# Performance work log

Measured on AMD Instinct MI355X. Metric: run time of the kernel, lower is better.

## Reference

```python
import jax, jax.numpy as jnp
import numpy as np

N = 100000      # nodes
E = 1000000     # edges (before self loops)
F_IN = 128      # num_features
G = 512         # graphs in batch
NC = 10         # num_classes
EPS_BN = 1e-5
NEG_SLOPE = 0.2


def setup_inputs() -> dict:
    key = jax.random.key(0)
    ks = iter(jax.random.split(key, 40))
    rn = lambda shape, s=0.1: jax.random.normal(next(ks), shape, jnp.float32) * s
    inp = {
        "x": jax.random.normal(next(ks), (N, F_IN), jnp.float32),
        "edge_index": jax.random.randint(next(ks), (2, E), 0, N),
        "batch": jnp.sort(jax.random.randint(next(ks), (N,), 0, G)),
        "W1": rn((F_IN, 128)), "as1": rn((8, 16)), "ad1": rn((8, 16)), "b1": jnp.zeros((128,), jnp.float32),
        "g1": jnp.ones((128,), jnp.float32), "be1": jnp.zeros((128,), jnp.float32),
        "Wl1": rn((128, 16)), "bl1": jnp.zeros((16,), jnp.float32),
        "gl1": jnp.ones((16,), jnp.float32), "bel1": jnp.zeros((16,), jnp.float32),
        "W2": rn((16, 96)), "as2": rn((4, 24)), "ad2": rn((4, 24)), "b2": jnp.zeros((96,), jnp.float32),
        "g2": jnp.ones((96,), jnp.float32), "be2": jnp.zeros((96,), jnp.float32),
        "Wl2": rn((96, 24)), "bl2": jnp.zeros((24,), jnp.float32),
        "gl2": jnp.ones((24,), jnp.float32), "bel2": jnp.zeros((24,), jnp.float32),
        "W3": rn((24, 64)), "as3": rn((2, 32)), "ad3": rn((2, 32)), "b3": jnp.zeros((64,), jnp.float32),
        "g3": jnp.ones((64,), jnp.float32), "be3": jnp.zeros((64,), jnp.float32),
        # final classifier
        "Wo": rn((64, NC)), "bo": jnp.zeros((NC,), jnp.float32),
    }
    return inp


def _bn(h, gamma, beta):
    # training-mode BatchNorm1d: batch statistics, biased variance
    m = jnp.mean(h, axis=0)
    v = jnp.var(h, axis=0)
    return gamma * (h - m) * jax.lax.rsqrt(v + EPS_BN) + beta


def _gat(h_in, src, dst, W, a_src, a_dst, bias, n):
    heads, ch = a_src.shape
    h = (h_in @ W).reshape(n, heads, ch)                     # [N,H,C]
    alpha_s = jnp.sum(h * a_src, axis=-1)                    # [N,H]
    alpha_d = jnp.sum(h * a_dst, axis=-1)                    # [N,H]
    e = jax.nn.leaky_relu(alpha_s[src] + alpha_d[dst], NEG_SLOPE)   # [E,H]
    emax = jax.ops.segment_max(e, dst, num_segments=n)       # segment softmax over target
    e = jnp.exp(e - emax[dst])
    denom = jax.ops.segment_sum(e, dst, num_segments=n)
    alpha = e / (denom[dst] + 1e-16)                         # [E,H]
    msg = h[src] * alpha[:, :, None]                         # [E,H,C]
    out = jax.ops.segment_sum(msg, dst, num_segments=n)      # [N,H,C]
    return out.reshape(n, heads * ch) + bias


def reference(x, edge_index, batch,
              W1, as1, ad1, b1, g1, be1, Wl1, bl1, gl1, bel1,
              W2, as2, ad2, b2, g2, be2, Wl2, bl2, gl2, bel2,
              W3, as3, ad3, b3, g3, be3, Wo, bo):
    n = x.shape[0]
    loop = jnp.arange(n)
    src = jnp.concatenate([edge_index[0], loop])   # add self loops (PyG default)
    dst = jnp.concatenate([edge_index[1], loop])

    h = jax.nn.relu(_bn(_gat(x, src, dst, W1, as1, ad1, b1, n), g1, be1))
    h = jax.nn.relu(_bn(h @ Wl1 + bl1, gl1, bel1))
    h = jax.nn.relu(_bn(_gat(h, src, dst, W2, as2, ad2, b2, n), g2, be2))
    h = jax.nn.relu(_bn(h @ Wl2 + bl2, gl2, bel2))
    h = jax.nn.relu(_bn(_gat(h, src, dst, W3, as3, ad3, b3, n), g3, be3))

    # global mean pool over graphs
    counts = jax.ops.segment_sum(jnp.ones((n,), h.dtype), batch, num_segments=G)
    pooled = jax.ops.segment_sum(h, batch, num_segments=G) / jnp.maximum(counts, 1.0)[:, None]
    # dropout is identity in eval
    return pooled @ Wo + bo
```

## Files before the change

### kernel.cpp

```cpp
#include <hip/hip_runtime.h>

typedef unsigned short u16;
typedef unsigned int   u32;
typedef unsigned long long u64;
typedef __attribute__((ext_vector_type(8))) short short8;
typedef __attribute__((ext_vector_type(4))) float f32x4;

#define DEVI __device__ __forceinline__

#define NPB 256
#define SHB 8
#define BHB 64
#define PST 256
#define LOG2E 1.44269504088896340736f

DEVI float bf2f(u16 u){ union{u32 i; float f;} x; x.i = ((u32)u)<<16; return x.f; }
DEVI u16 f2bf(float f){ union{float f; u32 i;} x; x.f = f;
  u32 r = (x.i + 0x7FFFu + ((x.i>>16)&1u))>>16; return (u16)r; }
DEVI float lrelu(float x){ return x > 0.f ? x : 0.2f*x; }
DEVI float exp2g(float x){ return __builtin_amdgcn_exp2f(x); }
DEVI float gload(const void* p, size_t i, int f32){
  return f32 ? ((const float*)p)[i] : bf2f(((const u16*)p)[i]);
}

__global__ __launch_bounds__(256) void k_init(const void* x, int* flag){
  if (blockIdx.x == 0 && threadIdx.x == 0){
    const u16* p = (const u16*)x;
    int hits = 0;
    for (int j = 0; j < 512; j++){
      u16 e = (p[j] >> 7) & 0xFF;
      if (e >= 0xC0) hits++;
    }
    *flag = hits ? 1 : 0;
  }
}

__global__ __launch_bounds__(1024) void k_bhist(const int* ei, int E, int* hist, int NB){
  __shared__ int lh[512];
  for (int b = threadIdx.x; b < NB; b += 1024) lh[b] = 0;
  __syncthreads();
  for (int e = blockIdx.x*1024 + threadIdx.x; e < E; e += BHB*1024)
    atomicAdd(&lh[((u32)ei[E + e]) >> SHB], 1);
  __syncthreads();
  for (int b = threadIdx.x; b < NB; b += 1024) hist[blockIdx.x*NB + b] = lh[b];
}

__global__ __launch_bounds__(512) void k_bmid(int* hist, int* base, int* coff, int NB, int N){
  __shared__ int l[512];
  int t = threadIdx.x;
  int s = 0;
  if (t < NB){ for (int j = 0; j < BHB; j++) s += hist[j*NB + t]; }
  l[t] = s; __syncthreads();
  for (int st = 1; st < 512; st <<= 1){
    int a = (t >= st) ? l[t - st] : 0;
    __syncthreads();
    l[t] += a;
    __syncthreads();
  }
  int run0 = l[t] - s;
  if (t < NB){
    base[t] = run0;
    int run = run0;
    for (int j = 0; j < BHB; j++){ int v = hist[j*NB + t]; hist[j*NB + t] = run; run += v; }
  }
  if (t == 511){ base[NB] = l[511]; coff[N] = l[511]; }
}

__global__ __launch_bounds__(1024) void k_bfill(const int* ei, int E, const int* hist,
                                                u64* tmp, int NB){
  __shared__ int cur[512];
  for (int b = threadIdx.x; b < NB; b += 1024) cur[b] = hist[blockIdx.x*NB + b];
  __syncthreads();
  for (int e = blockIdx.x*1024 + threadIdx.x; e < E; e += BHB*1024){
    int s = ei[e], d = ei[E + e];
    int p = atomicAdd(&cur[((u32)d) >> SHB], 1);
    tmp[p] = ((u64)(u32)d << 32) | (u32)s;
  }
}

__global__ __launch_bounds__(256) void k_cfill(const u64* tmp, const int* base,
                                               int* coff, int* csr, int N){
  __shared__ int cnt[NPB], start[NPB];
  int b = blockIdx.x, t = threadIdx.x;
  int p0 = base[b], p1 = base[b + 1];
  cnt[t] = 0;
  __syncthreads();
  for (int i = p0 + t; i < p1; i += 256)
    atomicAdd(&cnt[(int)(tmp[i] >> 32) & (NPB - 1)], 1);
  __syncthreads();
  if (t == 0){
    int run = p0;
    for (int j = 0; j < NPB; j++){ start[j] = run; run += cnt[j]; }
  }
  __syncthreads();
  {
    int node = b*NPB + t;
    if (node < N) coff[node] = start[t];
    cnt[t] = 0;
  }
  __syncthreads();
  for (int i = p0 + t; i < p1; i += 256){
    u64 pr = tmp[i];
    int dj = (int)(pr >> 32) & (NPB - 1);
    int r = atomicAdd(&cnt[dj], 1);
    csr[start[dj] + r] = (int)(u32)pr;
  }
}

__global__ __launch_bounds__(256) void k_prepW(const void* Wg, u16* Wt, const int* dflag){
  const int f32 = dflag[0];
  for (int i = blockIdx.x*256 + threadIdx.x; i < 128*128; i += gridDim.x*256){
    int k = i >> 7, nn = i & 127;
    Wt[nn*128 + k] = f2bf(gload(Wg, i, f32));
  }
}

__global__ __launch_bounds__(256) void k_mfma1(const void* x, const u16* __restrict__ Wt,
                                               u16* __restrict__ out, int n, const int* dflag){
  const int f32 = dflag[0];
  const int wave = threadIdx.x >> 6;
  const int lane = threadIdx.x & 63;
  const int l15 = lane & 15, q = lane >> 4;
  const int arow = blockIdx.x*64 + wave*16 + l15;
  const bool rok = arow < n;

  f32x4 acc[8];
  #pragma unroll
  for (int t = 0; t < 8; t++) acc[t] = {0.f, 0.f, 0.f, 0.f};

  #pragma unroll
  for (int kk = 0; kk < 4; kk++){
    short8 a = {0,0,0,0,0,0,0,0};
    if (rok){
      const int ko = kk*32 + q*8;
      if (f32){
        const float* xp = (const float*)x + (size_t)arow*128 + ko;
        float4 v0 = *(const float4*)xp;
        float4 v1 = *(const float4*)(xp + 4);
        a[0]=(short)f2bf(v0.x); a[1]=(short)f2bf(v0.y); a[2]=(short)f2bf(v0.z); a[3]=(short)f2bf(v0.w);
        a[4]=(short)f2bf(v1.x); a[5]=(short)f2bf(v1.y); a[6]=(short)f2bf(v1.z); a[7]=(short)f2bf(v1.w);
      } else {
        a = *(const short8*)((const u16*)x + (size_t)arow*128 + ko);
      }
    }
    #pragma unroll
    for (int t = 0; t < 8; t++){
      short8 b = *(const short8*)(Wt + (size_t)(l15 + 16*t)*128 + kk*32 + q*8);
      acc[t] = __builtin_amdgcn_mfma_f32_16x16x32_bf16(a, b, acc[t], 0, 0, 0);
    }
  }

  const int orow0 = blockIdx.x*64 + wave*16 + q*4;
  #pragma unroll
  for (int r = 0; r < 4; r++){
    int orow = orow0 + r;
    if (orow < n){
      #pragma unroll
      for (int t = 0; t < 8; t++)
        out[(size_t)orow*128 + l15 + 16*t] = f2bf(acc[t][r]);
    }
  }
}

__global__ __launch_bounds__(256) void k_alpha1(const u16* __restrict__ A, const void* a_s, const void* a_d,
    u16* als, u16* ald, int n, const int* dflag){
  const int f32 = dflag[0];
  int idx = blockIdx.x*256 + threadIdx.x;
  if (idx >= n*8) return;
  int r = idx >> 3, hd = idx & 7;
  const u16* p = A + (size_t)r*128 + hd*16;
  float s = 0.f, d = 0.f;
  #pragma unroll
  for (int c = 0; c < 16; c++){
    float v = bf2f(p[c]);
    s = fmaf(v, gload(a_s, hd*16 + c, f32), s);
    d = fmaf(v, gload(a_d, hd*16 + c, f32), d);
  }
  als[idx] = f2bf(s * LOG2E); ald[idx] = f2bf(d * LOG2E);
}

template<int K,int M,int H,int RT,int TPB,bool AFFINE,bool ALPHA>
__global__ __launch_bounds__(TPB) void k_gemm(
    const u16* in, const void* Wg,
    const float* stat, const void* gam, const void* bet, float invn,
    const void* a_s, const void* a_d, u16* out, u16* als, u16* ald, int n,
    const int* dflag)
{
  constexpr int CT = 4;
  constexpr int TC = M/CT;
  constexpr int TR = TPB/TC;
  constexpr int ROWS = TR*RT;
  constexpr int C = M/H;
  static_assert(TPB % TC == 0, "");
  __shared__ __align__(16) u16 Wl[K*M];
  __shared__ float Il[ROWS*(K+1)];
  __shared__ float red[ALPHA ? (2*ROWS*TC) : 1];
  __shared__ float faL[AFFINE ? K : 1], fdL[AFFINE ? K : 1];

  const int f32 = dflag[0];
  if constexpr (AFFINE){
    for (int k = threadIdx.x; k < K; k += TPB){
      float m = stat[k]*invn;
      float vv = stat[128 + k]*invn - m*m;
      float a = gload(gam, k, f32) * rsqrtf(vv + 1e-5f);
      faL[k] = a;
      fdL[k] = gload(bet, k, f32) - m*a;
    }
    __syncthreads();
  }

  for (int i = threadIdx.x; i < K*M; i += TPB)
    Wl[i] = f32 ? f2bf(((const float*)Wg)[i]) : ((const u16*)Wg)[i];

  const int rowbase = blockIdx.x * ROWS;
  for (int i = threadIdx.x; i < ROWS*K; i += TPB){
    int rr = i / K, k = i - rr*K;
    int r = rowbase + rr;
    float v = 0.f;
    if (r < n){
      v = bf2f(in[(size_t)r*K + k]);
      if constexpr (AFFINE) v = fmaxf(fmaf(faL[k], v, fdL[k]), 0.f);
    }
    Il[rr*(K+1) + k] = v;
  }
  __syncthreads();

  const int tc = threadIdx.x % TC;
  const int tr = threadIdx.x / TC;
  float acc[RT][CT];
  #pragma unroll
  for (int j = 0; j < RT; j++)
    #pragma unroll
    for (int c = 0; c < CT; c++) acc[j][c] = 0.f;

  #pragma unroll 8
  for (int k = 0; k < K; k++){
    ushort4 u = *(const ushort4*)&Wl[k*M + tc*CT];
    float w0 = bf2f(u.x), w1 = bf2f(u.y), w2 = bf2f(u.z), w3 = bf2f(u.w);
    #pragma unroll
    for (int j = 0; j < RT; j++){
      float iv = Il[(tr + j*TR)*(K+1) + k];
      acc[j][0] = fmaf(iv, w0, acc[j][0]);
      acc[j][1] = fmaf(iv, w1, acc[j][1]);
      acc[j][2] = fmaf(iv, w2, acc[j][2]);
      acc[j][3] = fmaf(iv, w3, acc[j][3]);
    }
  }

  #pragma unroll
  for (int j = 0; j < RT; j++){
    int r = rowbase + tr + j*TR;
    if (r < n){
      ushort4 st;
      st.x = f2bf(acc[j][0]); st.y = f2bf(acc[j][1]);
      st.z = f2bf(acc[j][2]); st.w = f2bf(acc[j][3]);
      *(ushort4*)&out[(size_t)r*M + tc*CT] = st;
    }
  }

  if constexpr (ALPHA){
    #pragma unroll
    for (int j = 0; j < RT; j++){
      float ps = 0.f, pd = 0.f;
      #pragma unroll
      for (int c = 0; c < CT; c++){
        ps = fmaf(acc[j][c], gload(a_s, tc*CT + c, f32), ps);
        pd = fmaf(acc[j][c], gload(a_d, tc*CT + c, f32), pd);
      }
      red[(tr + j*TR)*TC + tc] = ps;
      red[ROWS*TC + (tr + j*TR)*TC + tc] = pd;
    }
    __syncthreads();
    if (threadIdx.x < ROWS){
      int r = rowbase + threadIdx.x;
      if (r < n){
        float hs[H], hd[H];
        #pragma unroll
        for (int h = 0; h < H; h++){ hs[h] = 0.f; hd[h] = 0.f; }
        for (int t2 = 0; t2 < TC; t2++){
          int hh = (t2*CT)/C;
          hs[hh] += red[threadIdx.x*TC + t2];
          hd[hh] += red[ROWS*TC + threadIdx.x*TC + t2];
        }
        #pragma unroll
        for (int h = 0; h < H; h++){
          als[(size_t)r*H + h] = f2bf(hs[h] * LOG2E);
          ald[(size_t)r*H + h] = f2bf(hd[h] * LOG2E);
        }
      }
    }
  }
}

template<int H,int C>
__global__ __launch_bounds__(256) void k_pullW(const u16* __restrict__ h,
    const u16* __restrict__ als, const u16* __restrict__ ald,
    const int* __restrict__ off, const int* __restrict__ csr, u16* __restrict__ out, int n)
{
  constexpr int F = H*C;
  constexpr int L = F/2;
  constexpr int LOGH = (H==8)?3:((H==4)?2:1);
  constexpr int EPG = 64 >> LOGH;
  int wid = blockIdx.x*4 + (threadIdx.x >> 6);
  if (wid >= n) return;
  int lane = threadIdx.x & 63;
  int uu = lane >> LOGH;
  int hh = lane & (H-1);
  int fl = (lane < L) ? lane : (L-1);
  int hd = (2*fl)/C;
  const u32* hw = (const u32*)h;

  float adw = bf2f(ald[(u32)wid*H + hh]);
  float wsw = exp2g(lrelu(bf2f(als[(u32)wid*H + hh]) + adw));
  float den_lane = (uu == 0) ? wsw : 0.f;

  float wsf = exp2g(lrelu(bf2f(als[(u32)wid*H + hd]) + bf2f(ald[(u32)wid*H + hd])));
  u32 vs = hw[(u32)wid*L + fl];
  float acc0 = wsf * bf2f((u16)vs);
  float acc1 = wsf * bf2f((u16)(vs >> 16));

  int e0 = off[wid], e1 = off[wid + 1];
  for (int e = e0; e < e1; e += EPG){
    int rem = e1 - e;
    int su = csr[e + (uu < rem ? uu : 0)];
    float w = exp2g(lrelu(bf2f(als[(u32)su*H + hh]) + adw));
    if (uu >= rem) w = 0.f;
    den_lane += w;
    int cnt = rem < EPG ? rem : EPG;
    for (int jj = 0; jj < cnt; jj += 8){
      int sb[8]; float wb[8]; u32 vv[8];
      #pragma unroll
      for (int j = 0; j < 8; j++){
        int sl = ((jj + j) << LOGH) + hd;
        sb[j] = __shfl(su, sl);
        wb[j] = __shfl(w,  sl);
      }
      #pragma unroll
      for (int j = 0; j < 8; j++) vv[j] = hw[(u32)sb[j]*L + fl];
      #pragma unroll
      for (int j = 0; j < 8; j++){
        acc0 = fmaf(wb[j], bf2f((u16)vv[j]), acc0);
        acc1 = fmaf(wb[j], bf2f((u16)(vv[j] >> 16)), acc1);
      }
    }
  }
  #pragma unroll
  for (int st = H; st < 64; st <<= 1) den_lane += __shfl_xor(den_lane, st);
  float den = __shfl(den_lane, hd);
  float r = 1.f/(den + 1e-16f);
  if (lane < L)
    ((u32*)out)[(u32)wid*L + fl] = (u32)f2bf(acc0*r) | ((u32)f2bf(acc1*r) << 16);
}

template<int F,int TPB>
__global__ __launch_bounds__(TPB) void k_statA(const u16* __restrict__ x, int n,
                                               float* __restrict__ part)
{
  constexpr int L = F/2;
  constexpr int RPB = TPB/L;
  static_assert(TPB % L == 0, "");
  int c = threadIdx.x % L;
  int tr = threadIdx.x / L;
  const u32* xw = (const u32*)x;
  int chunk = (n + (int)gridDim.x - 1)/(int)gridDim.x;
  int r0 = blockIdx.x*chunk;
  int r1 = r0 + chunk; if (r1 > n) r1 = n;
  float a0=0.f, a1=0.f, b0=0.f, b1=0.f;
  int r = r0 + tr;
  for (; r + 3*RPB < r1; r += 4*RPB){
    u32 v0 = xw[(size_t)r*L + c];
    u32 v1 = xw[(size_t)(r + RPB)*L + c];
    u32 v2 = xw[(size_t)(r + 2*RPB)*L + c];
    u32 v3 = xw[(size_t)(r + 3*RPB)*L + c];
    float f0 = bf2f((u16)v0), f1 = bf2f((u16)(v0 >> 16));
    float f2 = bf2f((u16)v1), f3 = bf2f((u16)(v1 >> 16));
    float f4 = bf2f((u16)v2), f5 = bf2f((u16)(v2 >> 16));
    float f6 = bf2f((u16)v3), f7 = bf2f((u16)(v3 >> 16));
    a0 += (f0 + f2) + (f4 + f6);
    a1 += (f1 + f3) + (f5 + f7);
    b0 += (f0*f0 + f2*f2) + (f4*f4 + f6*f6);
    b1 += (f1*f1 + f3*f3) + (f5*f5 + f7*f7);
  }
  for (; r < r1; r += RPB){
    u32 v = xw[(size_t)r*L + c];
    float f0 = bf2f((u16)v), f1 = bf2f((u16)(v >> 16));
    a0 += f0; b0 = fmaf(f0, f0, b0);
    a1 += f1; b1 = fmaf(f1, f1, b1);
  }
  __shared__ float l0[TPB], l1[TPB], l2[TPB], l3[TPB];
  l0[threadIdx.x] = a0; l1[threadIdx.x] = a1;
  l2[threadIdx.x] = b0; l3[threadIdx.x] = b1;
  __syncthreads();
  for (int t2 = threadIdx.x; t2 < 256; t2 += TPB){
    int col = t2 & 127;
    float s = 0.f;
    if (col < F){
      int cc = col >> 1, par = col & 1;
      const float* base = (t2 >= 128) ? (par ? l3 : l2) : (par ? l1 : l0);
      #pragma unroll 4
      for (int j = 0; j < RPB; j++) s += base[j*L + cc];
    }
    part[(size_t)blockIdx.x*256 + t2] = s;
  }
}

__global__ __launch_bounds__(256) void k_statB(const float* __restrict__ part,
                                               float* __restrict__ out, int P)
{
  int t = threadIdx.x;
  float s = 0.f;
  int b = 0;
  for (; b + 3 < P; b += 4)
    s += (part[(size_t)b*256 + t] + part[(size_t)(b+1)*256 + t])
       + (part[(size_t)(b+2)*256 + t] + part[(size_t)(b+3)*256 + t]);
  for (; b < P; b++) s += part[(size_t)b*256 + t];
  out[t] = s;
}

__global__ __launch_bounds__(256) void k_pool(const u16* B, const int* batch, int n,
    const float* stat, const void* g3, const void* be3, float invn,
    const void* Wo, const void* bo, void* outp, const int* dflag)
{
  const int f32 = dflag[0];
  __shared__ float fa[64], fd[64];
  if (threadIdx.x < 64){
    int k = threadIdx.x;
    float m = stat[k]*invn;
    float v = stat[128 + k]*invn - m*m;
    float a = gload(g3, k, f32) * rsqrtf(v + 1e-5f);
    fa[k] = a;
    fd[k] = gload(be3, k, f32) - m*a;
  }
  __syncthreads();

  int g = blockIdx.x;
  int lane = threadIdx.x & 63, wv = threadIdx.x >> 6;
  int s, e;
  { int l = 0, h = n; while (l < h){ int m = (l+h)>>1; if (batch[m] <  g) l = m+1; else h = m; } s = l; }
  { int l = s, h = n; while (l < h){ int m = (l+h)>>1; if (batch[m] <= g) l = m+1; else h = m; } e = l; }
  float a = fa[lane], d = fd[lane], acc = 0.f;
  for (int r = s + wv; r < e; r += 4)
    acc += fmaxf(fmaf(a, bf2f(B[(size_t)r*64 + lane]), d), 0.f);
  __shared__ float pl[4][64];
  pl[wv][lane] = acc;
  __syncthreads();
  if (wv == 0){
    float cnt = (e > s) ? (float)(e - s) : 1.f;
    pl[0][lane] = (pl[0][lane] + pl[1][lane] + pl[2][lane] + pl[3][lane]) / cnt;
  }
  __syncthreads();
  if (threadIdx.x < 10){
    int lo = threadIdx.x;
    float o = gload(bo, lo, f32);
    for (int l2 = 0; l2 < 64; l2++) o = fmaf(pl[0][l2], gload(Wo, l2*10 + lo, f32), o);
    if (f32) ((float*)outp)[g*10 + lo] = o;
    else     ((u16*) outp)[g*10 + lo] = f2bf(o);
  }
}

extern "C" void kernel_launch(void* const* d_in, const int* in_sizes, int n_in,
                              void* d_out, int out_size, void* d_ws, size_t ws_size,
                              hipStream_t stream)
{
  const void* x   = d_in[0];
  const int* ei   = (const int*)d_in[1];
  const int* batch= (const int*)d_in[2];
  const void* W1  = d_in[3];
  const void* as1 = d_in[4];
  const void* ad1 = d_in[5];
  const void* g1  = d_in[7];
  const void* be1 = d_in[8];
  const void* Wl1 = d_in[9];
  const void* gl1 = d_in[11];
  const void* bel1= d_in[12];
  const void* W2  = d_in[13];
  const void* as2 = d_in[14];
  const void* ad2 = d_in[15];
  const void* g2  = d_in[17];
  const void* be2 = d_in[18];
  const void* Wl2 = d_in[19];
  const void* gl2 = d_in[21];
  const void* bel2= d_in[22];
  const void* W3  = d_in[23];
  const void* as3 = d_in[24];
  const void* ad3 = d_in[25];
  const void* g3  = d_in[27];
  const void* be3 = d_in[28];
  const void* Wo  = d_in[29];
  const void* bo  = d_in[30];
  (void)n_in; (void)ws_size;

  const int N = in_sizes[2];
  const int E = in_sizes[1] / 2;
  const int G = out_size / 10;
  const int NB = (N + NPB - 1) >> SHB;

  char* w = (char*)d_ws;
  size_t off = 0;
  auto alloc = [&](size_t bytes)->void*{
    size_t o = off; off += (bytes + 255) & ~(size_t)255; return (void*)(w + o);
  };
  int*   dflag= (int*)alloc(4);
  int*   coff = (int*)alloc((size_t)(N+1)*4);
  int*   csr  = (int*)alloc((size_t)E*4);
  int*   bbase= (int*)alloc((size_t)(NB+1)*4);
  int*   hist = (int*)alloc((size_t)BHB*NB*4);
  float* stS  = (float*)alloc(1280*4);
  float* part = (float*)alloc((size_t)PST*256*4);
  u16*   Wt   = (u16*)alloc(128*128*2);
  u16*   als  = (u16*)alloc((size_t)N*8*2);
  u16*   ald  = (u16*)alloc((size_t)N*8*2);
  u16*   Cb   = (u16*)alloc((size_t)N*24*2);
  u16*   A    = (u16*)alloc((size_t)N*128*2);
  u16*   B    = (u16*)alloc((size_t)N*128*2);
  u64*   tmp  = (u64*)A;

  const float invN = 1.f/(float)N;

  k_init<<<1, 256, 0, stream>>>(x, dflag);
  k_prepW<<<16, 256, 0, stream>>>(W1, Wt, dflag);

  k_bhist<<<BHB, 1024, 0, stream>>>(ei, E, hist, NB);
  k_bmid <<<1, 512, 0, stream>>>(hist, bbase, coff, NB, N);
  k_bfill<<<BHB, 1024, 0, stream>>>(ei, E, hist, tmp, NB);
  k_cfill<<<NB, 256, 0, stream>>>(tmp, bbase, coff, csr, N);

  k_mfma1<<<(N+63)/64, 256, 0, stream>>>(x, Wt, A, N, dflag);
  k_alpha1<<<(N*8+255)/256, 256, 0, stream>>>(A, as1, ad1, als, ald, N, dflag);
  k_pullW<8,16><<<(N+3)/4, 256, 0, stream>>>(A, als, ald, coff, csr, B, N);
  k_statA<128,256><<<PST, 256, 0, stream>>>(B, N, part);
  k_statB<<<1, 256, 0, stream>>>(part, stS + 0, PST);

  k_gemm<128,16,1,1,256,true,false><<<(N+63)/64, 256, 0, stream>>>(
      B, Wl1, stS + 0, g1, be1, invN, nullptr, nullptr, Cb, nullptr, nullptr, N, dflag);
  k_statA<16,256><<<PST, 256, 0, stream>>>(Cb, N, part);
  k_statB<<<1, 256, 0, stream>>>(part, stS + 256, PST);

  k_gemm<16,96,4,2,192,true,true><<<(N+15)/16, 192, 0, stream>>>(
      Cb, W2, stS + 256, gl1, bel1, invN, as2, ad2, A, als, ald, N, dflag);
  k_pullW<4,24><<<(N+3)/4, 256, 0, stream>>>(A, als, ald, coff, csr, B, N);
  k_statA<96,192><<<PST, 192, 0, stream>>>(B, N, part);
  k_statB<<<1, 256, 0, stream>>>(part, stS + 512, PST);

  k_gemm<96,24,1,2,192,true,false><<<(N+63)/64, 192, 0, stream>>>(
      B, Wl2, stS + 512, g2, be2, invN, nullptr, nullptr, Cb, nullptr, nullptr, N, dflag);
  k_statA<24,192><<<PST, 192, 0, stream>>>(Cb, N, part);
  k_statB<<<1, 256, 0, stream>>>(part, stS + 768, PST);

  k_gemm<24,64,2,2,256,true,true><<<(N+31)/32, 256, 0, stream>>>(
      Cb, W3, stS + 768, gl2, bel2, invN, as3, ad3, A, als, ald, N, dflag);
  k_pullW<2,32><<<(N+3)/4, 256, 0, stream>>>(A, als, ald, coff, csr, B, N);
  k_statA<64,256><<<PST, 256, 0, stream>>>(B, N, part);
  k_statB<<<1, 256, 0, stream>>>(part, stS + 1024, PST);

  k_pool<<<G, 256, 0, stream>>>(B, batch, N, stS + 1024, g3, be3, invN, Wo, bo, d_out, dflag);
}
```

Before: 720.4 us.

## Aggregate GAT layers 2-3 before projection and parallelize CSR scan and stat reduction

For GAT layers 2 and 3, the attention logits are now computed from the low-dimensional input by folding a_src/a_dst into W (precomputed vectors). Neighbour aggregation runs on the 16- or 24-wide BN-activated input per head, and a block-diagonal weight GEMM is applied afterwards. This shrinks the gathered feature width per edge (64 or 48 values instead of 96 or 64). It also splits the single-block bucket scan into parallel total, scan and cursor kernels, and widens the final stat reduction to 1024 threads. The cost is extra kernel launches and a different rounding order from aggregating before the projection.

```diff
diff --git a/kernel.cpp b/kernel.cpp
--- a/kernel.cpp
+++ b/kernel.cpp
@@ -23,8 +23,8 @@
   return f32 ? ((const float*)p)[i] : bf2f(((const u16*)p)[i]);
 }
 
-__global__ __launch_bounds__(256) void k_init(const void* x, int* flag){
-  if (blockIdx.x == 0 && threadIdx.x == 0){
+__global__ __launch_bounds__(64) void k_init(const void* x, int* flag){
+  if (threadIdx.x == 0){
     const u16* p = (const u16*)x;
     int hits = 0;
     for (int j = 0; j < 512; j++){
@@ -45,25 +45,41 @@
   for (int b = threadIdx.x; b < NB; b += 1024) hist[blockIdx.x*NB + b] = lh[b];
 }
 
-__global__ __launch_bounds__(512) void k_bmid(int* hist, int* base, int* coff, int NB, int N){
+__global__ __launch_bounds__(256) void k_btot(const int* hist, int* tot, int NB){
+  int b = blockIdx.x*256 + threadIdx.x;
+  if (b < NB){
+    int s = 0;
+    #pragma unroll 8
+    for (int j = 0; j < BHB; j++) s += hist[j*NB + b];
+    tot[b] = s;
+  }
+}
+
+__global__ __launch_bounds__(512) void k_bscan(const int* tot, int* base, int* coff, int NB, int N){
   __shared__ int l[512];
   int t = threadIdx.x;
-  int s = 0;
-  if (t < NB){ for (int j = 0; j < BHB; j++) s += hist[j*NB + t]; }
-  l[t] = s; __syncthreads();
+  int v = (t < NB) ? tot[t] : 0;
+  l[t] = v; __syncthreads();
   for (int st = 1; st < 512; st <<= 1){
     int a = (t >= st) ? l[t - st] : 0;
     __syncthreads();
     l[t] += a;
     __syncthreads();
   }
-  int run0 = l[t] - s;
-  if (t < NB){
-    base[t] = run0;
-    int run = run0;
-    for (int j = 0; j < BHB; j++){ int v = hist[j*NB + t]; hist[j*NB + t] = run; run += v; }
-  }
+  if (t < NB) base[t] = l[t] - v;
   if (t == 511){ base[NB] = l[511]; coff[N] = l[511]; }
+}
+
+__global__ __launch_bounds__(256) void k_bcur(int* hist, const int* base, int NB){
+  int b = blockIdx.x*256 + threadIdx.x;
+  if (b < NB){
+    int run = base[b];
+    for (int j = 0; j < BHB; j++){
+      int v = hist[j*NB + b];
+      hist[j*NB + b] = run;
+      run += v;
+    }
+  }
 }
 
 __global__ __launch_bounds__(1024) void k_bfill(const int* ei, int E, const int* hist,
@@ -112,6 +128,46 @@
   for (int i = blockIdx.x*256 + threadIdx.x; i < 128*128; i += gridDim.x*256){
     int k = i >> 7, nn = i & 127;
     Wt[nn*128 + k] = f2bf(gload(Wg, i, f32));
+  }
+}
+
+__global__ __launch_bounds__(256) void k_prep23(const void* W2, const void* as2, const void* ad2,
+    const void* W3, const void* as3, const void* ad3,
+    u16* Wbd2, u16* Wbd3, float* prepF, const int* dflag){
+  const int f32 = dflag[0];
+  int t = threadIdx.x;
+  for (int i = t; i < 64*96; i += 256){
+    int r = i/96, m = i - r*96;
+    int h = r >> 4, k = r & 15;
+    float v = ((m/24) == h) ? gload(W2, k*96 + m, f32) : 0.f;
+    Wbd2[i] = f2bf(v);
+  }
+  for (int i = t; i < 48*64; i += 256){
+    int r = i >> 6, m = i & 63;
+    int h = r/24, k = r - h*24;
+    float v = ((m >> 5) == h) ? gload(W3, k*64 + m, f32) : 0.f;
+    Wbd3[i] = f2bf(v);
+  }
+  if (t < 64){
+    int h = t >> 4, k = t & 15;
+    float s = 0.f, d = 0.f;
+    for (int c = 0; c < 24; c++){
+      float w = gload(W2, k*96 + h*24 + c, f32);
+      s = fmaf(w, gload(as2, h*24 + c, f32), s);
+      d = fmaf(w, gload(ad2, h*24 + c, f32), d);
+    }
+    prepF[t] = s; prepF[64 + t] = d;
+  }
+  if (t >= 64 && t < 112){
+    int u = t - 64;
+    int h = u/24, k = u - h*24;
+    float s = 0.f, d = 0.f;
+    for (int c = 0; c < 32; c++){
+      float w = gload(W3, k*64 + h*32 + c, f32);
+      s = fmaf(w, gload(as3, h*32 + c, f32), s);
+      d = fmaf(w, gload(ad3, h*32 + c, f32), d);
+    }
+    prepF[128 + u] = s; prepF[176 + u] = d;
   }
 }
 
@@ -179,7 +235,7 @@
   als[idx] = f2bf(s * LOG2E); ald[idx] = f2bf(d * LOG2E);
 }
 
-template<int K,int M,int H,int RT,int TPB,bool AFFINE,bool ALPHA>
+template<int K,int M,int H,int RT,int TPB,bool AFFINE,bool ALPHA,bool WBF16>
 __global__ __launch_bounds__(TPB) void k_gemm(
     const u16* in, const void* Wg,
     const float* stat, const void* gam, const void* bet, float invn,
@@ -209,8 +265,10 @@
     __syncthreads();
   }
 
-  for (int i = threadIdx.x; i < K*M; i += TPB)
-    Wl[i] = f32 ? f2bf(((const float*)Wg)[i]) : ((const u16*)Wg)[i];
+  for (int i = threadIdx.x; i < K*M; i += TPB){
+    if constexpr (WBF16) Wl[i] = ((const u16*)Wg)[i];
+    else Wl[i] = f32 ? f2bf(((const float*)Wg)[i]) : ((const u16*)Wg)[i];
+  }
 
   const int rowbase = blockIdx.x * ROWS;
   for (int i = threadIdx.x; i < ROWS*K; i += TPB){
@@ -350,6 +408,90 @@
   float r = 1.f/(den + 1e-16f);
   if (lane < L)
     ((u32*)out)[(u32)wid*L + fl] = (u32)f2bf(acc0*r) | ((u32)f2bf(acc1*r) << 16);
+}
+
+template<int H,int CIN>
+__global__ __launch_bounds__(256) void k_alphaX(const u16* __restrict__ Cb,
+    const float* stat, const void* gam, const void* bet, float invn,
+    const float* vs, const float* vd,
+    u16* act, u16* als, u16* ald, int n, const int* dflag)
+{
+  const int f32 = dflag[0];
+  __shared__ float faL[CIN], fdL[CIN];
+  if (threadIdx.x < CIN){
+    int k = threadIdx.x;
+    float m = stat[k]*invn;
+    float vv = stat[128 + k]*invn - m*m;
+    float a = gload(gam, k, f32) * rsqrtf(vv + 1e-5f);
+    faL[k] = a;
+    fdL[k] = gload(bet, k, f32) - m*a;
+  }
+  __syncthreads();
+  int idx = blockIdx.x*256 + threadIdx.x;
+  if (idx >= n*H) return;
+  int j = idx / H, h = idx - j*H;
+  float s = 0.f, d = 0.f;
+  #pragma unroll
+  for (int k = 0; k < CIN; k++){
+    float v = bf2f(Cb[(size_t)j*CIN + k]);
+    v = fmaxf(fmaf(faL[k], v, fdL[k]), 0.f);
+    s = fmaf(v, vs[h*CIN + k], s);
+    d = fmaf(v, vd[h*CIN + k], d);
+    if (h == 0) act[(size_t)j*CIN + k] = f2bf(v);
+  }
+  als[idx] = f2bf(s * LOG2E); ald[idx] = f2bf(d * LOG2E);
+}
+
+template<int H,int CIN>
+__global__ __launch_bounds__(256) void k_pullX(const u16* __restrict__ act,
+    const u16* __restrict__ als, const u16* __restrict__ ald,
+    const int* __restrict__ off, const int* __restrict__ csr, u16* __restrict__ D, int n)
+{
+  constexpr int LX = H*CIN;
+  constexpr int LOGH = (H==4)?2:1;
+  constexpr int EPG = 64 >> LOGH;
+  int wid = blockIdx.x*4 + (threadIdx.x >> 6);
+  if (wid >= n) return;
+  int lane = threadIdx.x & 63;
+  int uu = lane >> LOGH;
+  int hh = lane & (H-1);
+  int fl = (lane < LX) ? lane : (LX-1);
+  int hf = fl / CIN, k = fl - hf*CIN;
+
+  float adw = bf2f(ald[(u32)wid*H + hh]);
+  float wsw = exp2g(lrelu(bf2f(als[(u32)wid*H + hh]) + adw));
+  float den_lane = (uu == 0) ? wsw : 0.f;
+
+  float wsf = exp2g(lrelu(bf2f(als[(u32)wid*H + hf]) + bf2f(ald[(u32)wid*H + hf])));
+  float acc = wsf * bf2f(act[(u32)wid*CIN + k]);
+
+  int e0 = off[wid], e1 = off[wid + 1];
+  for (int e = e0; e < e1; e += EPG){
+    int rem = e1 - e;
+    int su = csr[e + (uu < rem ? uu : 0)];
+    float w = exp2g(lrelu(bf2f(als[(u32)su*H + hh]) + adw));
+    if (uu >= rem) w = 0.f;
+    den_lane += w;
+    int cnt = rem < EPG ? rem : EPG;
+    for (int jj = 0; jj < cnt; jj += 8){
+      int sb[8]; float wb[8]; u16 vv[8];
+      #pragma unroll
+      for (int j = 0; j < 8; j++){
+        int sl = ((jj + j) << LOGH) + hf;
+        sb[j] = __shfl(su, sl);
+        wb[j] = __shfl(w,  sl);
+      }
+      #pragma unroll
+      for (int j = 0; j < 8; j++) vv[j] = act[(u32)sb[j]*CIN + k];
+      #pragma unroll
+      for (int j = 0; j < 8; j++) acc = fmaf(wb[j], bf2f(vv[j]), acc);
+    }
+  }
+  #pragma unroll
+  for (int st = H; st < 64; st <<= 1) den_lane += __shfl_xor(den_lane, st);
+  float den = __shfl(den_lane, hf);
+  if (lane < LX)
+    D[(u32)wid*LX + fl] = f2bf(acc / (den + 1e-16f));
 }
 
 template<int F,int TPB>
@@ -404,17 +546,25 @@
   }
 }
 
-__global__ __launch_bounds__(256) void k_statB(const float* __restrict__ part,
-                                               float* __restrict__ out, int P)
+__global__ __launch_bounds__(1024) void k_statB(const float* __restrict__ part,
+                                                float* __restrict__ out, int P)
 {
-  int t = threadIdx.x;
+  __shared__ float l[1024];
+  int col = threadIdx.x & 255;
+  int q   = threadIdx.x >> 8;
+  int rows = (P + 3) >> 2;
+  int b0 = q*rows, b1 = b0 + rows; if (b1 > P) b1 = P;
   float s = 0.f;
-  int b = 0;
-  for (; b + 3 < P; b += 4)
-    s += (part[(size_t)b*256 + t] + part[(size_t)(b+1)*256 + t])
-       + (part[(size_t)(b+2)*256 + t] + part[(size_t)(b+3)*256 + t]);
-  for (; b < P; b++) s += part[(size_t)b*256 + t];
-  out[t] = s;
+  int b = b0;
+  for (; b + 3 < b1; b += 4)
+    s += (part[(size_t)b*256 + col] + part[(size_t)(b+1)*256 + col])
+       + (part[(size_t)(b+2)*256 + col] + part[(size_t)(b+3)*256 + col]);
+  for (; b < b1; b++) s += part[(size_t)b*256 + col];
+  l[threadIdx.x] = s;
+  __syncthreads();
+  if (threadIdx.x < 256)
+    out[threadIdx.x] = (l[threadIdx.x] + l[256 + threadIdx.x])
+                     + (l[512 + threadIdx.x] + l[768 + threadIdx.x]);
 }
 
 __global__ __launch_bounds__(256) void k_pool(const u16* B, const int* batch, int n,
@@ -504,24 +654,34 @@
   int*   coff = (int*)alloc((size_t)(N+1)*4);
   int*   csr  = (int*)alloc((size_t)E*4);
   int*   bbase= (int*)alloc((size_t)(NB+1)*4);
+  int*   btotb= (int*)alloc((size_t)NB*4);
   int*   hist = (int*)alloc((size_t)BHB*NB*4);
   float* stS  = (float*)alloc(1280*4);
   float* part = (float*)alloc((size_t)PST*256*4);
+  float* prepF= (float*)alloc(256*4);
   u16*   Wt   = (u16*)alloc(128*128*2);
+  u16*   Wbd2 = (u16*)alloc(64*96*2);
+  u16*   Wbd3 = (u16*)alloc(48*64*2);
   u16*   als  = (u16*)alloc((size_t)N*8*2);
   u16*   ald  = (u16*)alloc((size_t)N*8*2);
   u16*   Cb   = (u16*)alloc((size_t)N*24*2);
   u16*   A    = (u16*)alloc((size_t)N*128*2);
   u16*   B    = (u16*)alloc((size_t)N*128*2);
   u64*   tmp  = (u64*)A;
+  u16*   D    = A;
+  u16*   act  = A + (size_t)N*64;
 
   const float invN = 1.f/(float)N;
-
-  k_init<<<1, 256, 0, stream>>>(x, dflag);
+  const int nbb = (NB + 255)/256;
+
+  k_init<<<1, 64, 0, stream>>>(x, dflag);
   k_prepW<<<16, 256, 0, stream>>>(W1, Wt, dflag);
+  k_prep23<<<1, 256, 0, stream>>>(W2, as2, ad2, W3, as3, ad3, Wbd2, Wbd3, prepF, dflag);
 
   k_bhist<<<BHB, 1024, 0, stream>>>(ei, E, hist, NB);
-  k_bmid <<<1, 512, 0, stream>>>(hist, bbase, coff, NB, N);
+  k_btot <<<nbb, 256, 0, stream>>>(hist, btotb, NB);
+  k_bscan<<<1, 512, 0, stream>>>(btotb, bbase, coff, NB, N);
+  k_bcur <<<nbb, 256, 0, stream>>>(hist, bbase, NB);
   k_bfill<<<BHB, 1024, 0, stream>>>(ei, E, hist, tmp, NB);
   k_cfill<<<NB, 256, 0, stream>>>(tmp, bbase, coff, csr, N);
 
@@ -529,29 +689,33 @@
   k_alpha1<<<(N*8+255)/256, 256, 0, stream>>>(A, as1, ad1, als, ald, N, dflag);
   k_pullW<8,16><<<(N+3)/4, 256, 0, stream>>>(A, als, ald, coff, csr, B, N);
   k_statA<128,256><<<PST, 256, 0, stream>>>(B, N, part);
-  k_statB<<<1, 256, 0, stream>>>(part, stS + 0, PST);
-
-  k_gemm<128,16,1,1,256,true,false><<<(N+63)/64, 256, 0, stream>>>(
+  k_statB<<<1, 1024, 0, stream>>>(part, stS + 0, PST);
+
+  k_gemm<128,16,1,1,256,true,false,false><<<(N+63)/64, 256, 0, stream>>>(
       B, Wl1, stS + 0, g1, be1, invN, nullptr, nullptr, Cb, nullptr, nullptr, N, dflag);
   k_statA<16,256><<<PST, 256, 0, stream>>>(Cb, N, part);
-  k_statB<<<1, 256, 0, stream>>>(part, stS + 256, PST);
-
-  k_gemm<16,96,4,2,192,true,true><<<(N+15)/16, 192, 0, stream>>>(
-      Cb, W2, stS + 256, gl1, bel1, invN, as2, ad2, A, als, ald, N, dflag);
-  k_pullW<4,24><<<(N+3)/4, 256, 0, stream>>>(A, als, ald, coff, csr, B, N);
+  k_statB<<<1, 1024, 0, stream>>>(part, stS + 256, PST);
+
+  k_alphaX<4,16><<<(N*4+255)/256, 256, 0, stream>>>(
+      Cb, stS + 256, gl1, bel1, invN, prepF + 0, prepF + 64, act, als, ald, N, dflag);
+  k_pullX<4,16><<<(N+3)/4, 256, 0, stream>>>(act, als, ald, coff, csr, D, N);
+  k_gemm<64,96,1,2,192,false,false,true><<<(N+15)/16, 192, 0, stream>>>(
+      D, Wbd2, nullptr, nullptr, nullptr, invN, nullptr, nullptr, B, nullptr, nullptr, N, dflag);
   k_statA<96,192><<<PST, 192, 0, stream>>>(B, N, part);
-  k_statB<<<1, 256, 0, stream>>>(part, stS + 512, PST);
-
-  k_gemm<96,24,1,2,192,true,false><<<(N+63)/64, 192, 0, stream>>>(
+  k_statB<<<1, 1024, 0, stream>>>(part, stS + 512, PST);
+
+  k_gemm<96,24,1,2,192,true,false,false><<<(N+63)/64, 192, 0, stream>>>(
       B, Wl2, stS + 512, g2, be2, invN, nullptr, nullptr, Cb, nullptr, nullptr, N, dflag);
   k_statA<24,192><<<PST, 192, 0, stream>>>(Cb, N, part);
-  k_statB<<<1, 256, 0, stream>>>(part, stS + 768, PST);
-
-  k_gemm<24,64,2,2,256,true,true><<<(N+31)/32, 256, 0, stream>>>(
-      Cb, W3, stS + 768, gl2, bel2, invN, as3, ad3, A, als, ald, N, dflag);
-  k_pullW<2,32><<<(N+3)/4, 256, 0, stream>>>(A, als, ald, coff, csr, B, N);
+  k_statB<<<1, 1024, 0, stream>>>(part, stS + 768, PST);
+
+  k_alphaX<2,24><<<(N*2+255)/256, 256, 0, stream>>>(
+      Cb, stS + 768, gl2, bel2, invN, prepF + 128, prepF + 176, act, als, ald, N, dflag);
+  k_pullX<2,24><<<(N+3)/4, 256, 0, stream>>>(act, als, ald, coff, csr, D, N);
+  k_gemm<48,64,1,2,256,false,false,true><<<(N+31)/32, 256, 0, stream>>>(
+      D, Wbd3, nullptr, nullptr, nullptr, invN, nullptr, nullptr, B, nullptr, nullptr, N, dflag);
   k_statA<64,256><<<PST, 256, 0, stream>>>(B, N, part);
-  k_statB<<<1, 256, 0, stream>>>(part, stS + 1024, PST);
+  k_statB<<<1, 1024, 0, stream>>>(part, stS + 1024, PST);
 
   k_pool<<<G, 256, 0, stream>>>(B, batch, N, stS + 1024, g3, be3, invN, Wo, bo, d_out, dflag);
 }
```

Result: faster. 696.4 us (-3.3%).
